# Kernel optimization log

Measured on AMD Instinct MI355X. Metric: run time of the kernel, lower is better.

## Reference

```python
import jax, jax.numpy as jnp
import numpy as np

B, S, D, H = 4, 2048, 512, 8
HD = D // H  # head width = 64

def setup_inputs() -> dict:
    key = jax.random.key(0)
    ks = jax.random.split(key, 7)
    x = jax.random.normal(ks[0], (B, S, D), dtype=jnp.float32)
    mask = jnp.ones((B, S), dtype=jnp.int32)
    # torch nn.Linear(dim, dim): weight [out, in], bias [out]
    sc = 1.0 / np.sqrt(D)
    Wq = jax.random.uniform(ks[1], (D, D), jnp.float32, -sc, sc)
    bq = jax.random.uniform(ks[2], (D,), jnp.float32, -sc, sc)
    Wk = jax.random.uniform(ks[3], (D, D), jnp.float32, -sc, sc)
    bk = jax.random.uniform(ks[4], (D,), jnp.float32, -sc, sc)
    Wv = jax.random.uniform(ks[5], (D, D), jnp.float32, -sc, sc)
    bv = jax.random.uniform(ks[6], (D,), jnp.float32, -sc, sc)
    return {"x": x, "mask": mask, "Wq": Wq, "bq": bq, "Wk": Wk, "bk": bk, "Wv": Wv, "bv": bv}

def reference(x, mask, Wq, bq, Wk, bk, Wv, bv):
    # QKV projections (torch Linear: x @ W.T + b)
    q = jnp.einsum('bsd,ed->bse', x, Wq) + bq
    k = jnp.einsum('bsd,ed->bse', x, Wk) + bk
    v = jnp.einsum('bsd,ed->bse', x, Wv) + bv
    # split heads -> (B, H, S, HD)
    q = q.reshape(B, S, H, HD).transpose(0, 2, 1, 3)
    k = k.reshape(B, S, H, HD).transpose(0, 2, 1, 3)
    v = v.reshape(B, S, H, HD).transpose(0, 2, 1, 3)
    scores = jnp.einsum('bhqd,bhkd->bhqk', q, k) / np.sqrt(HD).astype(np.float32)
    m = mask[:, None, None, :].astype(scores.dtype)  # (B,1,1,S)
    scores = scores - 10000.0 * (1.0 - m)
    attn = jax.nn.softmax(scores, axis=-1)  # dropout is identity in eval mode
    h = jnp.einsum('bhqk,bhkd->bhqd', attn, v)
    h = h.transpose(0, 2, 1, 3).reshape(B, S, D)
    return h
```

## Files before the change

kernel.cpp:

```cpp
#include <hip/hip_runtime.h>
#include <hip/hip_bf16.h>

#define Bb 4
#define Ss 2048
#define Dd 512
#define Hh 8
#define HD 64
#define NX (Bb*Ss*Dd)
#define NW (3*Dd*Dd)

typedef __attribute__((ext_vector_type(8))) short bf8_t;
typedef __attribute__((ext_vector_type(4))) float f4_t;
typedef unsigned int u32;
typedef __attribute__((ext_vector_type(4))) unsigned int u32x4;

typedef const unsigned int __attribute__((address_space(1)))* gas_t;
typedef unsigned int __attribute__((address_space(3)))* las_t;

#define LOG2E 1.44269504088896f
#define MBIAS_C (-10000.0f * LOG2E)

__device__ __forceinline__ short cvt1(float f) {
  __hip_bfloat16 h = __float2bfloat16(f);
  union { __hip_bfloat16 hh; short ss; } u; u.hh = h; return u.ss;
}

__device__ __forceinline__ u32 pkrn(float a, float b) {
  union { __hip_bfloat162 h2; u32 u; } v;
  v.h2 = __float22bfloat162_rn(make_float2(a, b));
  return v.u;
}

__device__ __forceinline__ bf8_t pack8(float4 f0, float4 f1) {
  union { bf8_t v8; u32x4 u4; } u;
  u.u4.x = pkrn(f0.x, f0.y); u.u4.y = pkrn(f0.z, f0.w);
  u.u4.z = pkrn(f1.x, f1.y); u.u4.w = pkrn(f1.z, f1.w);
  return u.v8;
}

__device__ __forceinline__ void gload_lds16(const void* g, void* l) {
  __builtin_amdgcn_global_load_lds((gas_t)g, (las_t)l, 16, 0, 0);
}

__global__ __launch_bounds__(256) void convert_kernel(
    const float* __restrict__ x, const float* __restrict__ Wq,
    const float* __restrict__ Wk, const float* __restrict__ Wv,
    short* __restrict__ xb, short* __restrict__ Wb)
{
  size_t i = ((size_t)blockIdx.x * 256 + threadIdx.x) * 8;
  const float* src; short* dst;
  if (i < (size_t)NX) { src = x + i; dst = xb + i; }
  else {
    size_t j = i - NX;
    int ws = (int)(j >> 18);
    const float* W = (ws == 0) ? Wq : (ws == 1) ? Wk : Wv;
    src = W + (j & 0x3FFFF); dst = Wb + j;
  }
  float4 f0 = *(const float4*)src;
  float4 f1 = *(const float4*)(src + 4);
  *(bf8_t*)dst = pack8(f0, f1);
}

__global__ __launch_bounds__(256, 2) void qkv_proj_kernel(
    const short* __restrict__ xb, const short* __restrict__ Wb,
    const float* __restrict__ bq, const float* __restrict__ bk,
    const float* __restrict__ bv,
    short* __restrict__ Qg, short* __restrict__ Kg, short* __restrict__ Vtg)
{
  __shared__ short SM[32768];
  short* As0 = SM;
  short* Bs0 = SM + 16384;
  const int p = blockIdx.y >> 2;
  const short* __restrict__ W = Wb + (size_t)p * Dd * Dd;
  const float* __restrict__ bias = (p==0) ? bq : (p==1) ? bk : bv;
  const int m0 = blockIdx.x * 128;
  const int n0 = (blockIdx.y & 3) * 128;
  const int tid = threadIdx.x;
  const int lane = tid & 63, wid = tid >> 6;
  const int lq = lane & 15, hi = lane >> 4;
  const int wm = wid & 1, wn = wid >> 1;

  const short* aSrc[4];
  const short* bSrc[4];
  #pragma unroll
  for (int i = 0; i < 4; i++) {
    int slot = tid + i*256, row = slot >> 3, c = slot & 7;
    aSrc[i] = xb + (size_t)(m0 + row)*Dd + ((c ^ (row&7))*8);
    bSrc[i] = W  + (size_t)(n0 + row)*Dd + ((c ^ (row&7))*8);
  }

  int aoff[2][4], boff[2][4];
  #pragma unroll
  for (int ks = 0; ks < 2; ks++) {
    const int cu = ks*4 + hi;
    #pragma unroll
    for (int mi = 0; mi < 4; mi++) {
      int row = wm*64 + mi*16 + lq;
      aoff[ks][mi] = (row*64 + ((cu ^ (row&7))*8)) * 2;
    }
    #pragma unroll
    for (int nf = 0; nf < 4; nf++) {
      int row = wn*64 + nf*16 + lq;
      boff[ks][nf] = (row*64 + ((cu ^ (row&7))*8)) * 2;
    }
  }

  const f4_t zero4 = {0.f, 0.f, 0.f, 0.f};
  f4_t acc[4][4];
  #pragma unroll
  for (int i = 0; i < 4; i++)
    #pragma unroll
    for (int j = 0; j < 4; j++) acc[i][j] = zero4;

  auto STAGE = [&](int bufi, int k0) {
    #pragma unroll
    for (int i = 0; i < 4; i++) {
      gload_lds16(aSrc[i] + k0, As0 + bufi*8192 + (tid + i*256)*8);
      gload_lds16(bSrc[i] + k0, Bs0 + bufi*8192 + (tid + i*256)*8);
    }
  };

  STAGE(0, 0);
  __syncthreads();
  #pragma unroll 2
  for (int kt = 0; kt < 8; kt++) {
    const int cur = kt & 1;
    if (kt < 7) STAGE(cur ^ 1, (kt + 1)*64);
    const char* ab = (const char*)(As0 + cur*8192);
    const char* bbp = (const char*)(Bs0 + cur*8192);
    #pragma unroll
    for (int ks = 0; ks < 2; ks++) {
      bf8_t a[4], bfrag[4];
      #pragma unroll
      for (int mi = 0; mi < 4; mi++) a[mi] = *(const bf8_t*)(ab + aoff[ks][mi]);
      #pragma unroll
      for (int nf = 0; nf < 4; nf++) bfrag[nf] = *(const bf8_t*)(bbp + boff[ks][nf]);
      #pragma unroll
      for (int mi = 0; mi < 4; mi++)
        #pragma unroll
        for (int nf = 0; nf < 4; nf++)
          acc[mi][nf] = __builtin_amdgcn_mfma_f32_16x16x32_bf16(a[mi], bfrag[nf], acc[mi][nf], 0, 0, 0);
    }
    __syncthreads();
  }

  const float qs = (p == 0) ? 0.125f * LOG2E : 1.0f;
  float badd[4];
  #pragma unroll
  for (int nf = 0; nf < 4; nf++) badd[nf] = bias[n0 + wn*64 + nf*16 + lq];

  if (p == 2) {
    short* VL = SM;
    #pragma unroll
    for (int mi = 0; mi < 4; mi++)
      #pragma unroll
      for (int nf = 0; nf < 4; nf++) {
        const int colh = wn*64 + nf*16 + lq;
        #pragma unroll
        for (int r = 0; r < 4; r++) {
          int rowm = wm*64 + mi*16 + hi*4 + r;
          VL[colh*136 + rowm] = cvt1(acc[mi][nf][r] + badd[nf]);
        }
      }
    __syncthreads();
    const int row = tid >> 1, half = tid & 1;
    const int colg = n0 + row, hh = colg >> 6, hd = colg & 63;
    const int bb = m0 >> 11, ssb = (m0 & 2047) + half*64;
    short* dst = Vtg + (((size_t)bb*Hh + hh)*HD + hd)*Ss + ssb;
    const short* src = VL + row*136 + half*64;
    #pragma unroll
    for (int j = 0; j < 8; j++)
      *(bf8_t*)(dst + j*8) = *(const bf8_t*)(src + j*8);
  } else {
    #pragma unroll
    for (int mi = 0; mi < 4; mi++) {
      #pragma unroll
      for (int nf = 0; nf < 4; nf++) {
        const int col = n0 + wn*64 + nf*16 + lq;
        const int h = col >> 6, hd = col & 63;
        #pragma unroll
        for (int r = 0; r < 4; r++) {
          int mrow = m0 + wm*64 + mi*16 + hi*4 + r;
          int bb = mrow >> 11, ss = mrow & (Ss-1);
          short val = cvt1((acc[mi][nf][r] + badd[nf]) * qs);
          if (p == 0)
            Qg[(((size_t)bb*Hh + h)*Ss + ss)*HD + hd] = val;
          else
            Kg[(((size_t)bb*Hh + h)*Ss + ss)*HD + hd] = val;
        }
      }
    }
  }
}

__global__ __launch_bounds__(256, 2) void attn_kernel(
    const short* __restrict__ Qg, const short* __restrict__ Kg,
    const short* __restrict__ Vtg, const int* __restrict__ mask,
    float* __restrict__ out)
{
  __shared__ short Ks[2][64*64];
  __shared__ short Vs[2][64*64];
  const int bh = blockIdx.x;
  const int b = bh >> 3, h = bh & 7;
  const int tid = threadIdx.x, lane = tid & 63, w = tid >> 6;
  const int hi = lane >> 4, lq = lane & 15, tau = hi & 1;
  const short* __restrict__ Qb = Qg + (size_t)bh * Ss * HD;
  const short* __restrict__ Kb = Kg + (size_t)bh * Ss * HD;
  const short* __restrict__ Vb = Vtg + (size_t)bh * HD * Ss;
  const int* __restrict__ maskb = mask + b * Ss;
  const int q0 = blockIdx.y * 128 + w * 32;
  const int NT = Ss / 64;

  u32 mvbits = 0;
  #pragma unroll
  for (int t = 0; t < NT; t++)
    mvbits |= (maskb[t*64 + lane] != 0 ? 1u : 0u) << t;

  bf8_t qf[2][2];
  #pragma unroll
  for (int qg = 0; qg < 2; qg++)
    #pragma unroll
    for (int ks = 0; ks < 2; ks++)
      qf[qg][ks] = *(const bf8_t*)(Qb + (size_t)(q0 + qg*16 + lq)*HD + ks*32 + hi*8);

  int koffs[4][2], voffs[4][2];
  #pragma unroll
  for (int kb = 0; kb < 4; kb++) {
    int row = kb*16 + lq;
    #pragma unroll
    for (int ks = 0; ks < 2; ks++)
      koffs[kb][ks] = (row*64 + ((ks*4 + hi) ^ (row&7))*8) * 2;
  }
  #pragma unroll
  for (int nf2 = 0; nf2 < 4; nf2++) {
    int vr = nf2*16 + lq;
    #pragma unroll
    for (int ks2 = 0; ks2 < 2; ks2++)
      voffs[nf2][ks2] = (vr*64 + ((ks2*4 + hi) ^ (vr&7))*8) * 2;
  }

  const f4_t zero4 = {0.f, 0.f, 0.f, 0.f};
  f4_t o0[4], o1[4];
  #pragma unroll
  for (int j = 0; j < 4; j++) { o0[j] = zero4; o1[j] = zero4; }
  f4_t lacc0 = zero4, lacc1 = zero4;

  const bf8_t ones = {(short)0x3F80,(short)0x3F80,(short)0x3F80,(short)0x3F80,
                      (short)0x3F80,(short)0x3F80,(short)0x3F80,(short)0x3F80};

  const int sA = tid, sB = tid + 256;
  const short* ksrcA = Kb + (size_t)(sA>>3)*HD + (((sA&7) ^ ((sA>>3)&7))*8);
  const short* ksrcB = Kb + (size_t)(sB>>3)*HD + (((sB&7) ^ ((sB>>3)&7))*8);
  const short* vsrcA = Vb + (size_t)(sA>>3)*Ss + (((sA&7) ^ ((sA>>3)&7))*8);
  const short* vsrcB = Vb + (size_t)(sB>>3)*Ss + (((sB&7) ^ ((sB>>3)&7))*8);

  auto STAGE = [&](int bufi, int kv) {
    gload_lds16(ksrcA + (size_t)kv*HD, &Ks[bufi][sA*8]);
    gload_lds16(ksrcB + (size_t)kv*HD, &Ks[bufi][sB*8]);
    gload_lds16(vsrcA + kv,            &Vs[bufi][sA*8]);
    gload_lds16(vsrcB + kv,            &Vs[bufi][sB*8]);
  };

  STAGE(0, 0);
  __syncthreads();
  #pragma unroll 2
  for (int t = 0; t < NT; t++) {
    const int cur = t & 1;
    if (t + 1 < NT) STAGE(cur ^ 1, (t + 1)*64);
    const char* kbase = (const char*)&Ks[cur][0];
    const char* vbase = (const char*)&Vs[cur][0];

    f4_t sa[4], sb[4];
    #pragma unroll
    for (int kb = 0; kb < 4; kb++) {
      bf8_t kf0 = *(const bf8_t*)(kbase + koffs[kb][0]);
      bf8_t kf1 = *(const bf8_t*)(kbase + koffs[kb][1]);
      sa[kb] = __builtin_amdgcn_mfma_f32_16x16x32_bf16(kf0, qf[0][0], zero4, 0, 0, 0);
      sa[kb] = __builtin_amdgcn_mfma_f32_16x16x32_bf16(kf1, qf[0][1], sa[kb], 0, 0, 0);
      sb[kb] = __builtin_amdgcn_mfma_f32_16x16x32_bf16(kf0, qf[1][0], zero4, 0, 0, 0);
      sb[kb] = __builtin_amdgcn_mfma_f32_16x16x32_bf16(kf1, qf[1][1], sb[kb], 0, 0, 0);
    }
    const bool mok = (mvbits >> t) & 1u;
    if (__any(!mok)) {
      float mbl = mok ? 0.0f : MBIAS_C;
      #pragma unroll
      for (int kb = 0; kb < 4; kb++)
        #pragma unroll
        for (int r = 0; r < 4; r++) {
          float mm = __shfl(mbl, kb*16 + hi*4 + r, 64);
          sa[kb][r] += mm; sb[kb][r] += mm;
        }
    }
    bf8_t pf0[2], pf1[2];
    {
      u32 Wa[4][2], Wbp[4][2];
      #pragma unroll
      for (int kb = 0; kb < 4; kb++) {
        Wa[kb][0] = pkrn(__builtin_amdgcn_exp2f(sa[kb][0]), __builtin_amdgcn_exp2f(sa[kb][1]));
        Wa[kb][1] = pkrn(__builtin_amdgcn_exp2f(sa[kb][2]), __builtin_amdgcn_exp2f(sa[kb][3]));
        Wbp[kb][0] = pkrn(__builtin_amdgcn_exp2f(sb[kb][0]), __builtin_amdgcn_exp2f(sb[kb][1]));
        Wbp[kb][1] = pkrn(__builtin_amdgcn_exp2f(sb[kb][2]), __builtin_amdgcn_exp2f(sb[kb][3]));
      }
      #pragma unroll
      for (int c = 0; c < 2; c++) {
        u32 ma[4], mb[4];
        #pragma unroll
        for (int d = 0; d < 2; d++) {
          u32 X = Wa[2*c][d], Y = Wa[2*c+1][d];
          asm volatile("v_permlane32_swap_b32 %0, %1" : "+v"(X), "+v"(Y));
          u32 Xs = (u32)__builtin_amdgcn_ds_swizzle((int)X, 0x401F);
          u32 Ys = (u32)__builtin_amdgcn_ds_swizzle((int)Y, 0x401F);
          ma[d]     = tau ? Ys : X;
          ma[2 + d] = tau ? Y  : Xs;
          u32 X2 = Wbp[2*c][d], Y2 = Wbp[2*c+1][d];
          asm volatile("v_permlane32_swap_b32 %0, %1" : "+v"(X2), "+v"(Y2));
          u32 X2s = (u32)__builtin_amdgcn_ds_swizzle((int)X2, 0x401F);
          u32 Y2s = (u32)__builtin_amdgcn_ds_swizzle((int)Y2, 0x401F);
          mb[d]     = tau ? Y2s : X2;
          mb[2 + d] = tau ? Y2  : X2s;
        }
        union { bf8_t v8; u32x4 u4; } pa, pb;
        pa.u4.x = ma[0]; pa.u4.y = ma[1]; pa.u4.z = ma[2]; pa.u4.w = ma[3];
        pb.u4.x = mb[0]; pb.u4.y = mb[1]; pb.u4.z = mb[2]; pb.u4.w = mb[3];
        pf0[c] = pa.v8; pf1[c] = pb.v8;
      }
    }
    __builtin_amdgcn_s_setprio(1);
    lacc0 = __builtin_amdgcn_mfma_f32_16x16x32_bf16(pf0[0], ones, lacc0, 0, 0, 0);
    lacc0 = __builtin_amdgcn_mfma_f32_16x16x32_bf16(pf0[1], ones, lacc0, 0, 0, 0);
    lacc1 = __builtin_amdgcn_mfma_f32_16x16x32_bf16(pf1[0], ones, lacc1, 0, 0, 0);
    lacc1 = __builtin_amdgcn_mfma_f32_16x16x32_bf16(pf1[1], ones, lacc1, 0, 0, 0);
    #pragma unroll
    for (int nf2 = 0; nf2 < 4; nf2++) {
      #pragma unroll
      for (int ks2 = 0; ks2 < 2; ks2++) {
        bf8_t vf = *(const bf8_t*)(vbase + voffs[nf2][ks2]);
        o0[nf2] = __builtin_amdgcn_mfma_f32_16x16x32_bf16(pf0[ks2], vf, o0[nf2], 0, 0, 0);
        o1[nf2] = __builtin_amdgcn_mfma_f32_16x16x32_bf16(pf1[ks2], vf, o1[nf2], 0, 0, 0);
      }
    }
    __builtin_amdgcn_s_setprio(0);
    __syncthreads();
  }

  #pragma unroll
  for (int nf2 = 0; nf2 < 4; nf2++)
    #pragma unroll
    for (int r = 0; r < 4; r++) {
      int srow0 = q0 + hi*4 + r;
      int srow1 = q0 + 16 + hi*4 + r;
      out[((size_t)(b*Ss + srow0))*Dd + h*HD + nf2*16 + lq] = o0[nf2][r] / lacc0[r];
      out[((size_t)(b*Ss + srow1))*Dd + h*HD + nf2*16 + lq] = o1[nf2][r] / lacc1[r];
    }
}

extern "C" void kernel_launch(void* const* d_in, const int* in_sizes, int n_in,
                              void* d_out, int out_size, void* d_ws, size_t ws_size,
                              hipStream_t stream) {
  const float* x  = (const float*)d_in[0];
  const int* mask = (const int*)d_in[1];
  const float* Wq = (const float*)d_in[2];
  const float* bq = (const float*)d_in[3];
  const float* Wk = (const float*)d_in[4];
  const float* bk = (const float*)d_in[5];
  const float* Wv = (const float*)d_in[6];
  const float* bv = (const float*)d_in[7];
  float* out = (float*)d_out;

  short* Qg = (short*)d_ws;
  short* Kg = Qg + (size_t)Bb*Hh*Ss*HD;
  short* Vt = Kg + (size_t)Bb*Hh*Ss*HD;
  short* xb = Vt + (size_t)Bb*Hh*Ss*HD;
  short* Wb = xb + (size_t)NX;

  convert_kernel<<<dim3((NX + NW)/2048), 256, 0, stream>>>(x, Wq, Wk, Wv, xb, Wb);
  qkv_proj_kernel<<<dim3(64, 12), 256, 0, stream>>>(xb, Wb, bq, bk, bv, Qg, Kg, Vt);
  attn_kernel<<<dim3(32, 16), 256, 0, stream>>>(Qg, Kg, Vt, mask, out);
}
```

Baseline: 80.36 us.

## Split key range across two wave groups in attention block and merge via LDS

The attention kernel now launches 512 threads per block, arranged as two groups of four waves. Each group processes half of the key/value sequence with its own double-buffered LDS tiles. Afterwards the second group writes its partial outputs and row sums into shared memory, and the first group adds them and normalizes. This halves the serial KV loop per wave and doubles the waves resident per query tile, to hide latency better. The cost is more LDS per block, an extra reduction phase, and a merge that assumes no running-max rescaling is needed.

```diff
diff --git a/kernel.cpp b/kernel.cpp
--- a/kernel.cpp
+++ b/kernel.cpp
@@ -193,28 +193,33 @@
   }
 }
 
-__global__ __launch_bounds__(256, 2) void attn_kernel(
+__global__ __launch_bounds__(512, 4) void attn_kernel(
     const short* __restrict__ Qg, const short* __restrict__ Kg,
     const short* __restrict__ Vtg, const int* __restrict__ mask,
     float* __restrict__ out)
 {
-  __shared__ short Ks[2][64*64];
-  __shared__ short Vs[2][64*64];
+  __shared__ short SM[32768];
+  __shared__ float lex[4][32];
   const int bh = blockIdx.x;
   const int b = bh >> 3, h = bh & 7;
   const int tid = threadIdx.x, lane = tid & 63, w = tid >> 6;
+  const int g = w >> 2, wg = w & 3, gtid = tid & 255;
   const int hi = lane >> 4, lq = lane & 15, tau = hi & 1;
   const short* __restrict__ Qb = Qg + (size_t)bh * Ss * HD;
   const short* __restrict__ Kb = Kg + (size_t)bh * Ss * HD;
   const short* __restrict__ Vb = Vtg + (size_t)bh * HD * Ss;
   const int* __restrict__ maskb = mask + b * Ss;
-  const int q0 = blockIdx.y * 128 + w * 32;
-  const int NT = Ss / 64;
+  const int q0 = blockIdx.y * 128 + wg * 32;
+  const int koff = g << 10;
+  const int NT2 = 16;
+
+  short* gK = SM + g*16384;
+  short* gV = SM + g*16384 + 8192;
 
   u32 mvbits = 0;
   #pragma unroll
-  for (int t = 0; t < NT; t++)
-    mvbits |= (maskb[t*64 + lane] != 0 ? 1u : 0u) << t;
+  for (int t = 0; t < NT2; t++)
+    mvbits |= (maskb[koff + t*64 + lane] != 0 ? 1u : 0u) << t;
 
   bf8_t qf[2][2];
   #pragma unroll
@@ -248,27 +253,27 @@
   const bf8_t ones = {(short)0x3F80,(short)0x3F80,(short)0x3F80,(short)0x3F80,
                       (short)0x3F80,(short)0x3F80,(short)0x3F80,(short)0x3F80};
 
-  const int sA = tid, sB = tid + 256;
+  const int sA = gtid, sB = gtid + 256;
   const short* ksrcA = Kb + (size_t)(sA>>3)*HD + (((sA&7) ^ ((sA>>3)&7))*8);
   const short* ksrcB = Kb + (size_t)(sB>>3)*HD + (((sB&7) ^ ((sB>>3)&7))*8);
   const short* vsrcA = Vb + (size_t)(sA>>3)*Ss + (((sA&7) ^ ((sA>>3)&7))*8);
   const short* vsrcB = Vb + (size_t)(sB>>3)*Ss + (((sB&7) ^ ((sB>>3)&7))*8);
 
   auto STAGE = [&](int bufi, int kv) {
-    gload_lds16(ksrcA + (size_t)kv*HD, &Ks[bufi][sA*8]);
-    gload_lds16(ksrcB + (size_t)kv*HD, &Ks[bufi][sB*8]);
-    gload_lds16(vsrcA + kv,            &Vs[bufi][sA*8]);
-    gload_lds16(vsrcB + kv,            &Vs[bufi][sB*8]);
+    gload_lds16(ksrcA + (size_t)kv*HD, gK + bufi*4096 + sA*8);
+    gload_lds16(ksrcB + (size_t)kv*HD, gK + bufi*4096 + sB*8);
+    gload_lds16(vsrcA + kv,            gV + bufi*4096 + sA*8);
+    gload_lds16(vsrcB + kv,            gV + bufi*4096 + sB*8);
   };
 
-  STAGE(0, 0);
+  STAGE(0, koff);
   __syncthreads();
   #pragma unroll 2
-  for (int t = 0; t < NT; t++) {
+  for (int t = 0; t < NT2; t++) {
     const int cur = t & 1;
-    if (t + 1 < NT) STAGE(cur ^ 1, (t + 1)*64);
-    const char* kbase = (const char*)&Ks[cur][0];
-    const char* vbase = (const char*)&Vs[cur][0];
+    if (t + 1 < NT2) STAGE(cur ^ 1, koff + (t + 1)*64);
+    const char* kbase = (const char*)(gK + cur*4096);
+    const char* vbase = (const char*)(gV + cur*4096);
 
     f4_t sa[4], sb[4];
     #pragma unroll
@@ -343,15 +348,44 @@
     __syncthreads();
   }
 
-  #pragma unroll
-  for (int nf2 = 0; nf2 < 4; nf2++)
+  float* OX = (float*)(SM + 16384);
+  if (g == 1) {
+    float* myOX = OX + wg*2048;
+    #pragma unroll
+    for (int nf2 = 0; nf2 < 4; nf2++)
+      #pragma unroll
+      for (int r = 0; r < 4; r++) {
+        myOX[(hi*4 + r)*64 + nf2*16 + lq]        = o0[nf2][r];
+        myOX[1024 + (hi*4 + r)*64 + nf2*16 + lq] = o1[nf2][r];
+      }
+    if (lq == 0) {
+      #pragma unroll
+      for (int r = 0; r < 4; r++) {
+        lex[wg][hi*4 + r]      = lacc0[r];
+        lex[wg][16 + hi*4 + r] = lacc1[r];
+      }
+    }
+  }
+  __syncthreads();
+  if (g == 0) {
+    const float* pOX = OX + wg*2048;
     #pragma unroll
     for (int r = 0; r < 4; r++) {
-      int srow0 = q0 + hi*4 + r;
-      int srow1 = q0 + 16 + hi*4 + r;
-      out[((size_t)(b*Ss + srow0))*Dd + h*HD + nf2*16 + lq] = o0[nf2][r] / lacc0[r];
-      out[((size_t)(b*Ss + srow1))*Dd + h*HD + nf2*16 + lq] = o1[nf2][r] / lacc1[r];
-    }
+      lacc0[r] += lex[wg][hi*4 + r];
+      lacc1[r] += lex[wg][16 + hi*4 + r];
+    }
+    #pragma unroll
+    for (int nf2 = 0; nf2 < 4; nf2++)
+      #pragma unroll
+      for (int r = 0; r < 4; r++) {
+        float v0 = o0[nf2][r] + pOX[(hi*4 + r)*64 + nf2*16 + lq];
+        float v1 = o1[nf2][r] + pOX[1024 + (hi*4 + r)*64 + nf2*16 + lq];
+        int srow0 = q0 + hi*4 + r;
+        int srow1 = q0 + 16 + hi*4 + r;
+        out[((size_t)(b*Ss + srow0))*Dd + h*HD + nf2*16 + lq] = v0 / lacc0[r];
+        out[((size_t)(b*Ss + srow1))*Dd + h*HD + nf2*16 + lq] = v1 / lacc1[r];
+      }
+  }
 }
 
 extern "C" void kernel_launch(void* const* d_in, const int* in_sizes, int n_in,
@@ -375,5 +409,5 @@
 
   convert_kernel<<<dim3((NX + NW)/2048), 256, 0, stream>>>(x, Wq, Wk, Wv, xb, Wb);
   qkv_proj_kernel<<<dim3(64, 12), 256, 0, stream>>>(xb, Wb, bq, bk, bv, Qg, Kg, Vt);
-  attn_kernel<<<dim3(32, 16), 256, 0, stream>>>(Qg, Kg, Vt, mask, out);
-}
+  attn_kernel<<<dim3(32, 16), 512, 0, stream>>>(Qg, Kg, Vt, mask, out);
+}
```

Result: no change. 79.81 us (-0.7%).

## Fuse x bf16 conversion into QKV GEMM and widen attention KV tiles

Applied to the files above, without the earlier changes.

The separate conversion pass over x is removed. The QKV projection kernel now loads fp32 x into registers, packs it to bf16, and writes it into LDS after the MFMA work for the current stage, which removes a full round trip of x through global memory. Weight conversion stays as its own small kernel. Separately, the attention kernel now stages 128 keys per pipeline step as two 64-wide sub-tiles, which halves the number of barriers and stage issues but doubles LDS use per block and adds register pressure.

```diff
diff --git a/kernel.cpp b/kernel.cpp
--- a/kernel.cpp
+++ b/kernel.cpp
@@ -42,27 +42,21 @@
   __builtin_amdgcn_global_load_lds((gas_t)g, (las_t)l, 16, 0, 0);
 }
 
-__global__ __launch_bounds__(256) void convert_kernel(
-    const float* __restrict__ x, const float* __restrict__ Wq,
-    const float* __restrict__ Wk, const float* __restrict__ Wv,
-    short* __restrict__ xb, short* __restrict__ Wb)
+__global__ __launch_bounds__(256) void convertW_kernel(
+    const float* __restrict__ Wq, const float* __restrict__ Wk,
+    const float* __restrict__ Wv, short* __restrict__ Wb)
 {
-  size_t i = ((size_t)blockIdx.x * 256 + threadIdx.x) * 8;
-  const float* src; short* dst;
-  if (i < (size_t)NX) { src = x + i; dst = xb + i; }
-  else {
-    size_t j = i - NX;
-    int ws = (int)(j >> 18);
-    const float* W = (ws == 0) ? Wq : (ws == 1) ? Wk : Wv;
-    src = W + (j & 0x3FFFF); dst = Wb + j;
-  }
+  size_t j = ((size_t)blockIdx.x * 256 + threadIdx.x) * 8;
+  int ws = (int)(j >> 18);
+  const float* W = (ws == 0) ? Wq : (ws == 1) ? Wk : Wv;
+  const float* src = W + (j & 0x3FFFF);
   float4 f0 = *(const float4*)src;
   float4 f1 = *(const float4*)(src + 4);
-  *(bf8_t*)dst = pack8(f0, f1);
+  *(bf8_t*)(Wb + j) = pack8(f0, f1);
 }
 
 __global__ __launch_bounds__(256, 2) void qkv_proj_kernel(
-    const short* __restrict__ xb, const short* __restrict__ Wb,
+    const float* __restrict__ x, const short* __restrict__ Wb,
     const float* __restrict__ bq, const float* __restrict__ bk,
     const float* __restrict__ bv,
     short* __restrict__ Qg, short* __restrict__ Kg, short* __restrict__ Vtg)
@@ -80,12 +74,14 @@
   const int lq = lane & 15, hi = lane >> 4;
   const int wm = wid & 1, wn = wid >> 1;
 
-  const short* aSrc[4];
+  const float* xSrc[4];
   const short* bSrc[4];
+  int slotArr[4];
   #pragma unroll
   for (int i = 0; i < 4; i++) {
     int slot = tid + i*256, row = slot >> 3, c = slot & 7;
-    aSrc[i] = xb + (size_t)(m0 + row)*Dd + ((c ^ (row&7))*8);
+    slotArr[i] = slot;
+    xSrc[i] = x  + (size_t)(m0 + row)*Dd + ((c ^ (row&7))*8);
     bSrc[i] = W  + (size_t)(n0 + row)*Dd + ((c ^ (row&7))*8);
   }
 
@@ -112,20 +108,32 @@
     #pragma unroll
     for (int j = 0; j < 4; j++) acc[i][j] = zero4;
 
-  auto STAGE = [&](int bufi, int k0) {
+  float4 xr[4][2];
+  auto LOADX = [&](int k0) {
     #pragma unroll
     for (int i = 0; i < 4; i++) {
-      gload_lds16(aSrc[i] + k0, As0 + bufi*8192 + (tid + i*256)*8);
-      gload_lds16(bSrc[i] + k0, Bs0 + bufi*8192 + (tid + i*256)*8);
+      xr[i][0] = *(const float4*)(xSrc[i] + k0);
+      xr[i][1] = *(const float4*)(xSrc[i] + k0 + 4);
     }
   };
-
-  STAGE(0, 0);
+  auto WRITEX = [&](int bufi) {
+    #pragma unroll
+    for (int i = 0; i < 4; i++)
+      *(bf8_t*)(As0 + bufi*8192 + slotArr[i]*8) = pack8(xr[i][0], xr[i][1]);
+  };
+  auto GLOADW = [&](int bufi, int k0) {
+    #pragma unroll
+    for (int i = 0; i < 4; i++)
+      gload_lds16(bSrc[i] + k0, Bs0 + bufi*8192 + slotArr[i]*8);
+  };
+
+  LOADX(0); GLOADW(0, 0);
+  WRITEX(0);
   __syncthreads();
   #pragma unroll 2
   for (int kt = 0; kt < 8; kt++) {
     const int cur = kt & 1;
-    if (kt < 7) STAGE(cur ^ 1, (kt + 1)*64);
+    if (kt < 7) { LOADX((kt + 1)*64); GLOADW(cur ^ 1, (kt + 1)*64); }
     const char* ab = (const char*)(As0 + cur*8192);
     const char* bbp = (const char*)(Bs0 + cur*8192);
     #pragma unroll
@@ -141,6 +149,7 @@
         for (int nf = 0; nf < 4; nf++)
           acc[mi][nf] = __builtin_amdgcn_mfma_f32_16x16x32_bf16(a[mi], bfrag[nf], acc[mi][nf], 0, 0, 0);
     }
+    if (kt < 7) WRITEX(cur ^ 1);
     __syncthreads();
   }
 
@@ -198,8 +207,8 @@
     const short* __restrict__ Vtg, const int* __restrict__ mask,
     float* __restrict__ out)
 {
-  __shared__ short Ks[2][64*64];
-  __shared__ short Vs[2][64*64];
+  __shared__ short Ks[2][128*64];
+  __shared__ short Vs[2][2][64*64];
   const int bh = blockIdx.x;
   const int b = bh >> 3, h = bh & 7;
   const int tid = threadIdx.x, lane = tid & 63, w = tid >> 6;
@@ -209,11 +218,11 @@
   const short* __restrict__ Vb = Vtg + (size_t)bh * HD * Ss;
   const int* __restrict__ maskb = mask + b * Ss;
   const int q0 = blockIdx.y * 128 + w * 32;
-  const int NT = Ss / 64;
+  const int NT = Ss / 128;
 
   u32 mvbits = 0;
   #pragma unroll
-  for (int t = 0; t < NT; t++)
+  for (int t = 0; t < 32; t++)
     mvbits |= (maskb[t*64 + lane] != 0 ? 1u : 0u) << t;
 
   bf8_t qf[2][2];
@@ -248,17 +257,27 @@
   const bf8_t ones = {(short)0x3F80,(short)0x3F80,(short)0x3F80,(short)0x3F80,
                       (short)0x3F80,(short)0x3F80,(short)0x3F80,(short)0x3F80};
 
-  const int sA = tid, sB = tid + 256;
-  const short* ksrcA = Kb + (size_t)(sA>>3)*HD + (((sA&7) ^ ((sA>>3)&7))*8);
-  const short* ksrcB = Kb + (size_t)(sB>>3)*HD + (((sB&7) ^ ((sB>>3)&7))*8);
-  const short* vsrcA = Vb + (size_t)(sA>>3)*Ss + (((sA&7) ^ ((sA>>3)&7))*8);
-  const short* vsrcB = Vb + (size_t)(sB>>3)*Ss + (((sB&7) ^ ((sB>>3)&7))*8);
+  const short* ksrcS[4];
+  const short* vsrcS[4];
+  int kslot[4], vslot[4];
+  #pragma unroll
+  for (int i = 0; i < 4; i++) {
+    int s = tid + i*256;
+    kslot[i] = s;
+    int krow = s >> 3, kc = s & 7;
+    ksrcS[i] = Kb + (size_t)krow*HD + ((kc ^ (krow&7))*8);
+    vslot[i] = s;
+    int vrow = (s >> 3) & 63, vc = s & 7;
+    vsrcS[i] = Vb + (size_t)vrow*Ss + ((vc ^ (vrow&7))*8) + (s >> 9)*64;
+  }
 
   auto STAGE = [&](int bufi, int kv) {
-    gload_lds16(ksrcA + (size_t)kv*HD, &Ks[bufi][sA*8]);
-    gload_lds16(ksrcB + (size_t)kv*HD, &Ks[bufi][sB*8]);
-    gload_lds16(vsrcA + kv,            &Vs[bufi][sA*8]);
-    gload_lds16(vsrcB + kv,            &Vs[bufi][sB*8]);
+    #pragma unroll
+    for (int i = 0; i < 4; i++)
+      gload_lds16(ksrcS[i] + (size_t)kv*HD, &Ks[bufi][kslot[i]*8]);
+    #pragma unroll
+    for (int i = 0; i < 4; i++)
+      gload_lds16(vsrcS[i] + kv, &Vs[bufi][0][vslot[i]*8]);
   };
 
   STAGE(0, 0);
@@ -266,80 +285,83 @@
   #pragma unroll 2
   for (int t = 0; t < NT; t++) {
     const int cur = t & 1;
-    if (t + 1 < NT) STAGE(cur ^ 1, (t + 1)*64);
-    const char* kbase = (const char*)&Ks[cur][0];
-    const char* vbase = (const char*)&Vs[cur][0];
-
-    f4_t sa[4], sb[4];
-    #pragma unroll
-    for (int kb = 0; kb < 4; kb++) {
-      bf8_t kf0 = *(const bf8_t*)(kbase + koffs[kb][0]);
-      bf8_t kf1 = *(const bf8_t*)(kbase + koffs[kb][1]);
-      sa[kb] = __builtin_amdgcn_mfma_f32_16x16x32_bf16(kf0, qf[0][0], zero4, 0, 0, 0);
-      sa[kb] = __builtin_amdgcn_mfma_f32_16x16x32_bf16(kf1, qf[0][1], sa[kb], 0, 0, 0);
-      sb[kb] = __builtin_amdgcn_mfma_f32_16x16x32_bf16(kf0, qf[1][0], zero4, 0, 0, 0);
-      sb[kb] = __builtin_amdgcn_mfma_f32_16x16x32_bf16(kf1, qf[1][1], sb[kb], 0, 0, 0);
-    }
-    const bool mok = (mvbits >> t) & 1u;
-    if (__any(!mok)) {
-      float mbl = mok ? 0.0f : MBIAS_C;
-      #pragma unroll
-      for (int kb = 0; kb < 4; kb++)
-        #pragma unroll
-        for (int r = 0; r < 4; r++) {
-          float mm = __shfl(mbl, kb*16 + hi*4 + r, 64);
-          sa[kb][r] += mm; sb[kb][r] += mm;
+    if (t + 1 < NT) STAGE(cur ^ 1, (t + 1)*128);
+    #pragma unroll
+    for (int p = 0; p < 2; p++) {
+      const char* kbase = (const char*)&Ks[cur][0] + p*8192;
+      const char* vbase = (const char*)&Vs[cur][p][0];
+
+      f4_t sa[4], sb[4];
+      #pragma unroll
+      for (int kb = 0; kb < 4; kb++) {
+        bf8_t kf0 = *(const bf8_t*)(kbase + koffs[kb][0]);
+        bf8_t kf1 = *(const bf8_t*)(kbase + koffs[kb][1]);
+        sa[kb] = __builtin_amdgcn_mfma_f32_16x16x32_bf16(kf0, qf[0][0], zero4, 0, 0, 0);
+        sa[kb] = __builtin_amdgcn_mfma_f32_16x16x32_bf16(kf1, qf[0][1], sa[kb], 0, 0, 0);
+        sb[kb] = __builtin_amdgcn_mfma_f32_16x16x32_bf16(kf0, qf[1][0], zero4, 0, 0, 0);
+        sb[kb] = __builtin_amdgcn_mfma_f32_16x16x32_bf16(kf1, qf[1][1], sb[kb], 0, 0, 0);
+      }
+      const bool mok = (mvbits >> (t*2 + p)) & 1u;
+      if (__any(!mok)) {
+        float mbl = mok ? 0.0f : MBIAS_C;
+        #pragma unroll
+        for (int kb = 0; kb < 4; kb++)
+          #pragma unroll
+          for (int r = 0; r < 4; r++) {
+            float mm = __shfl(mbl, kb*16 + hi*4 + r, 64);
+            sa[kb][r] += mm; sb[kb][r] += mm;
+          }
+      }
+      bf8_t pf0[2], pf1[2];
+      {
+        u32 Wa[4][2], Wbp[4][2];
+        #pragma unroll
+        for (int kb = 0; kb < 4; kb++) {
+          Wa[kb][0] = pkrn(__builtin_amdgcn_exp2f(sa[kb][0]), __builtin_amdgcn_exp2f(sa[kb][1]));
+          Wa[kb][1] = pkrn(__builtin_amdgcn_exp2f(sa[kb][2]), __builtin_amdgcn_exp2f(sa[kb][3]));
+          Wbp[kb][0] = pkrn(__builtin_amdgcn_exp2f(sb[kb][0]), __builtin_amdgcn_exp2f(sb[kb][1]));
+          Wbp[kb][1] = pkrn(__builtin_amdgcn_exp2f(sb[kb][2]), __builtin_amdgcn_exp2f(sb[kb][3]));
         }
-    }
-    bf8_t pf0[2], pf1[2];
-    {
-      u32 Wa[4][2], Wbp[4][2];
-      #pragma unroll
-      for (int kb = 0; kb < 4; kb++) {
-        Wa[kb][0] = pkrn(__builtin_amdgcn_exp2f(sa[kb][0]), __builtin_amdgcn_exp2f(sa[kb][1]));
-        Wa[kb][1] = pkrn(__builtin_amdgcn_exp2f(sa[kb][2]), __builtin_amdgcn_exp2f(sa[kb][3]));
-        Wbp[kb][0] = pkrn(__builtin_amdgcn_exp2f(sb[kb][0]), __builtin_amdgcn_exp2f(sb[kb][1]));
-        Wbp[kb][1] = pkrn(__builtin_amdgcn_exp2f(sb[kb][2]), __builtin_amdgcn_exp2f(sb[kb][3]));
-      }
-      #pragma unroll
-      for (int c = 0; c < 2; c++) {
-        u32 ma[4], mb[4];
-        #pragma unroll
-        for (int d = 0; d < 2; d++) {
-          u32 X = Wa[2*c][d], Y = Wa[2*c+1][d];
-          asm volatile("v_permlane32_swap_b32 %0, %1" : "+v"(X), "+v"(Y));
-          u32 Xs = (u32)__builtin_amdgcn_ds_swizzle((int)X, 0x401F);
-          u32 Ys = (u32)__builtin_amdgcn_ds_swizzle((int)Y, 0x401F);
-          ma[d]     = tau ? Ys : X;
-          ma[2 + d] = tau ? Y  : Xs;
-          u32 X2 = Wbp[2*c][d], Y2 = Wbp[2*c+1][d];
-          asm volatile("v_permlane32_swap_b32 %0, %1" : "+v"(X2), "+v"(Y2));
-          u32 X2s = (u32)__builtin_amdgcn_ds_swizzle((int)X2, 0x401F);
-          u32 Y2s = (u32)__builtin_amdgcn_ds_swizzle((int)Y2, 0x401F);
-          mb[d]     = tau ? Y2s : X2;
-          mb[2 + d] = tau ? Y2  : X2s;
+        #pragma unroll
+        for (int c = 0; c < 2; c++) {
+          u32 ma[4], mb[4];
+          #pragma unroll
+          for (int d = 0; d < 2; d++) {
+            u32 X = Wa[2*c][d], Y = Wa[2*c+1][d];
+            asm volatile("v_permlane32_swap_b32 %0, %1" : "+v"(X), "+v"(Y));
+            u32 Xs = (u32)__builtin_amdgcn_ds_swizzle((int)X, 0x401F);
+            u32 Ys = (u32)__builtin_amdgcn_ds_swizzle((int)Y, 0x401F);
+            ma[d]     = tau ? Ys : X;
+            ma[2 + d] = tau ? Y  : Xs;
+            u32 X2 = Wbp[2*c][d], Y2 = Wbp[2*c+1][d];
+            asm volatile("v_permlane32_swap_b32 %0, %1" : "+v"(X2), "+v"(Y2));
+            u32 X2s = (u32)__builtin_amdgcn_ds_swizzle((int)X2, 0x401F);
+            u32 Y2s = (u32)__builtin_amdgcn_ds_swizzle((int)Y2, 0x401F);
+            mb[d]     = tau ? Y2s : X2;
+            mb[2 + d] = tau ? Y2  : X2s;
+          }
+          union { bf8_t v8; u32x4 u4; } pa, pb;
+          pa.u4.x = ma[0]; pa.u4.y = ma[1]; pa.u4.z = ma[2]; pa.u4.w = ma[3];
+          pb.u4.x = mb[0]; pb.u4.y = mb[1]; pb.u4.z = mb[2]; pb.u4.w = mb[3];
+          pf0[c] = pa.v8; pf1[c] = pb.v8;
         }
-        union { bf8_t v8; u32x4 u4; } pa, pb;
-        pa.u4.x = ma[0]; pa.u4.y = ma[1]; pa.u4.z = ma[2]; pa.u4.w = ma[3];
-        pb.u4.x = mb[0]; pb.u4.y = mb[1]; pb.u4.z = mb[2]; pb.u4.w = mb[3];
-        pf0[c] = pa.v8; pf1[c] = pb.v8;
-      }
-    }
-    __builtin_amdgcn_s_setprio(1);
-    lacc0 = __builtin_amdgcn_mfma_f32_16x16x32_bf16(pf0[0], ones, lacc0, 0, 0, 0);
-    lacc0 = __builtin_amdgcn_mfma_f32_16x16x32_bf16(pf0[1], ones, lacc0, 0, 0, 0);
-    lacc1 = __builtin_amdgcn_mfma_f32_16x16x32_bf16(pf1[0], ones, lacc1, 0, 0, 0);
-    lacc1 = __builtin_amdgcn_mfma_f32_16x16x32_bf16(pf1[1], ones, lacc1, 0, 0, 0);
-    #pragma unroll
-    for (int nf2 = 0; nf2 < 4; nf2++) {
-      #pragma unroll
-      for (int ks2 = 0; ks2 < 2; ks2++) {
-        bf8_t vf = *(const bf8_t*)(vbase + voffs[nf2][ks2]);
-        o0[nf2] = __builtin_amdgcn_mfma_f32_16x16x32_bf16(pf0[ks2], vf, o0[nf2], 0, 0, 0);
-        o1[nf2] = __builtin_amdgcn_mfma_f32_16x16x32_bf16(pf1[ks2], vf, o1[nf2], 0, 0, 0);
-      }
-    }
-    __builtin_amdgcn_s_setprio(0);
+      }
+      __builtin_amdgcn_s_setprio(1);
+      lacc0 = __builtin_amdgcn_mfma_f32_16x16x32_bf16(pf0[0], ones, lacc0, 0, 0, 0);
+      lacc0 = __builtin_amdgcn_mfma_f32_16x16x32_bf16(pf0[1], ones, lacc0, 0, 0, 0);
+      lacc1 = __builtin_amdgcn_mfma_f32_16x16x32_bf16(pf1[0], ones, lacc1, 0, 0, 0);
+      lacc1 = __builtin_amdgcn_mfma_f32_16x16x32_bf16(pf1[1], ones, lacc1, 0, 0, 0);
+      #pragma unroll
+      for (int nf2 = 0; nf2 < 4; nf2++) {
+        #pragma unroll
+        for (int ks2 = 0; ks2 < 2; ks2++) {
+          bf8_t vf = *(const bf8_t*)(vbase + voffs[nf2][ks2]);
+          o0[nf2] = __builtin_amdgcn_mfma_f32_16x16x32_bf16(pf0[ks2], vf, o0[nf2], 0, 0, 0);
+          o1[nf2] = __builtin_amdgcn_mfma_f32_16x16x32_bf16(pf1[ks2], vf, o1[nf2], 0, 0, 0);
+        }
+      }
+      __builtin_amdgcn_s_setprio(0);
+    }
     __syncthreads();
   }
 
@@ -370,10 +392,9 @@
   short* Qg = (short*)d_ws;
   short* Kg = Qg + (size_t)Bb*Hh*Ss*HD;
   short* Vt = Kg + (size_t)Bb*Hh*Ss*HD;
-  short* xb = Vt + (size_t)Bb*Hh*Ss*HD;
-  short* Wb = xb + (size_t)NX;
-
-  convert_kernel<<<dim3((NX + NW)/2048), 256, 0, stream>>>(x, Wq, Wk, Wv, xb, Wb);
-  qkv_proj_kernel<<<dim3(64, 12), 256, 0, stream>>>(xb, Wb, bq, bk, bv, Qg, Kg, Vt);
+  short* Wb = Vt + (size_t)Bb*Hh*Ss*HD;
+
+  convertW_kernel<<<dim3(NW/2048), 256, 0, stream>>>(Wq, Wk, Wv, Wb);
+  qkv_proj_kernel<<<dim3(64, 12), 256, 0, stream>>>(x, Wb, bq, bk, bv, Qg, Kg, Vt);
   attn_kernel<<<dim3(32, 16), 256, 0, stream>>>(Qg, Kg, Vt, mask, out);
 }
```

Result: slower. 82.57 us (+2.7%).
